# Optimization experiments

Measured on AMD Instinct MI355X. Metric: run time of the kernel, lower is better.

Reference implementation:

```python
import jax, jax.numpy as jnp
import numpy as np

B, H, N, D = 1, 1, 4096, 1024
DFF = 4096
LN_EPS = 1e-5


def _layer_norm(x, g, b):
    m = jnp.mean(x, axis=-1, keepdims=True)
    v = jnp.mean(jnp.square(x - m), axis=-1, keepdims=True)
    return (x - m) * jax.lax.rsqrt(v + LN_EPS) * g + b


def _mha(q, k, v, W, b):
    # NOTE: source has no 1/sqrt(d) scaling -- kept faithful.
    a = jnp.einsum('bhnd,bhmd->bhnm', q, k)
    a = jax.nn.softmax(a, axis=-1)
    o = jnp.einsum('bhnm,bhmd->bhnd', a, v)
    bb, hh, nn, dd = o.shape
    o = o.transpose(0, 2, 1, 3).reshape(bb, nn, hh * dd)  # b n (h d)
    return o @ W.T + b


def setup_inputs() -> dict:
    key = jax.random.key(0)
    ks = jax.random.split(key, 16)
    s = 0.02
    return {
        'x': jax.random.normal(ks[0], (B, H, N, D), jnp.float32),
        'x_encoder': jax.random.normal(ks[1], (B, H, N, D), jnp.float32),
        'pos': jax.random.normal(ks[2], (B, H, N, D), jnp.float32),
        'query_pos': jax.random.normal(ks[3], (B, H, N, D), jnp.float32),
        'Wp_sa': jax.random.normal(ks[4], (D, D), jnp.float32) * s,
        'bp_sa': jnp.zeros((D,), jnp.float32),
        'Wp_ca': jax.random.normal(ks[5], (D, D), jnp.float32) * s,
        'bp_ca': jnp.zeros((D,), jnp.float32),
        'W1': jax.random.normal(ks[6], (DFF, D), jnp.float32) * s,
        'b1': jnp.zeros((DFF,), jnp.float32),
        'W2': jax.random.normal(ks[7], (D, DFF), jnp.float32) * s,
        'b2': jnp.zeros((D,), jnp.float32),
        'g_sa': jnp.ones((D,), jnp.float32),
        'be_sa': jnp.zeros((D,), jnp.float32),
        'g_ca': jnp.ones((D,), jnp.float32),
        'be_ca': jnp.zeros((D,), jnp.float32),
        'g_ff': jnp.ones((D,), jnp.float32),
        'be_ff': jnp.zeros((D,), jnp.float32),
    }


def reference(x, x_encoder, pos, query_pos, Wp_sa, bp_sa, Wp_ca, bp_ca,
              W1, b1, W2, b2, g_sa, be_sa, g_ca, be_ca, g_ff, be_ff):
    # self-attention block
    n1 = _layer_norm(x, g_sa, be_sa)
    qk = n1 + pos
    x = _mha(qk, qk, n1, Wp_sa, bp_sa) + x
    # cross-attention block
    n2 = _layer_norm(x, g_ca, be_ca)
    q = n2 + query_pos
    k = x_encoder + pos
    x = _mha(q, k, x_encoder, Wp_ca, bp_ca) + x
    # feed-forward block (exact GELU, matching torch nn.GELU default)
    n3 = _layer_norm(x, g_ff, be_ff)
    h = jax.nn.gelu(n3 @ W1.T + b1, approximate=False)
    x = (h @ W2.T + b2) + x
    return x
```

## Files before the change

kernel.cpp:

```cpp
#include <hip/hip_runtime.h>
#include <hip/hip_fp16.h>
#include <cstdint>
#include <cstdio>

#define NROW 4096
#define DMODEL 1024
#define DFF_ 4096

typedef _Float16 f16;
typedef _Float16 f16x4 __attribute__((ext_vector_type(4)));
typedef _Float16 f16x8 __attribute__((ext_vector_type(8)));
typedef float f32x4 __attribute__((ext_vector_type(4)));

__device__ __forceinline__ void g2l16(const void* g, void* l) {
  __builtin_amdgcn_global_load_lds((const __attribute__((address_space(1))) void*)g,
                                   (__attribute__((address_space(3))) void*)l,
                                   16, 0, 0);
}

__device__ __forceinline__ int xcd_swz16() {
  const int bid = blockIdx.y * gridDim.x + blockIdx.x;
  const int nwg = gridDim.x * gridDim.y;
  return (bid & 7) * (nwg >> 3) + (bid >> 3);
}

__global__ __launch_bounds__(256) void cvt_f32_f16(const float* __restrict__ in,
                                                   f16* __restrict__ out, long n4) {
  for (long i = (long)blockIdx.x * blockDim.x + threadIdx.x; i < n4;
       i += (long)gridDim.x * blockDim.x) {
    float4 a = ((const float4*)in)[i];
    f16x4 h = {(f16)a.x, (f16)a.y, (f16)a.z, (f16)a.w};
    ((f16x4*)out)[i] = h;
  }
}

__global__ __launch_bounds__(256) void add_cvt(const float* __restrict__ xe,
                                               const float* __restrict__ pos,
                                               f16* __restrict__ k16,
                                               f16* __restrict__ xe16, long n4) {
  for (long i = (long)blockIdx.x * blockDim.x + threadIdx.x; i < n4;
       i += (long)gridDim.x * blockDim.x) {
    float4 a = ((const float4*)xe)[i];
    float4 p = ((const float4*)pos)[i];
    f16x4 k = {(f16)(a.x + p.x), (f16)(a.y + p.y), (f16)(a.z + p.z), (f16)(a.w + p.w)};
    f16x4 v = {(f16)a.x, (f16)a.y, (f16)a.z, (f16)a.w};
    ((f16x4*)k16)[i] = k;
    ((f16x4*)xe16)[i] = v;
  }
}

__global__ __launch_bounds__(256) void ln_row(const float* __restrict__ x,
                                              const float* __restrict__ g,
                                              const float* __restrict__ b,
                                              const float* __restrict__ pos,
                                              f16* __restrict__ nout,
                                              f16* __restrict__ qout) {
  const int row = blockIdx.x, tid = threadIdx.x;
  const float4 xv = ((const float4*)(x + (long)row * DMODEL))[tid];
  float s = xv.x + xv.y + xv.z + xv.w;
  float ss = xv.x * xv.x + xv.y * xv.y + xv.z * xv.z + xv.w * xv.w;
  for (int o = 32; o; o >>= 1) { s += __shfl_xor(s, o); ss += __shfl_xor(ss, o); }
  __shared__ float rs[4], rss[4];
  const int wid = tid >> 6, lane = tid & 63;
  if (!lane) { rs[wid] = s; rss[wid] = ss; }
  __syncthreads();
  s = rs[0] + rs[1] + rs[2] + rs[3];
  ss = rss[0] + rss[1] + rss[2] + rss[3];
  const float mean = s * (1.f / DMODEL);
  const float var = ss * (1.f / DMODEL) - mean * mean;
  const float rstd = rsqrtf(var + 1e-5f);
  const float4 gv = ((const float4*)g)[tid];
  const float4 bv = ((const float4*)b)[tid];
  float4 nv;
  nv.x = (xv.x - mean) * rstd * gv.x + bv.x;
  nv.y = (xv.y - mean) * rstd * gv.y + bv.y;
  nv.z = (xv.z - mean) * rstd * gv.z + bv.z;
  nv.w = (xv.w - mean) * rstd * gv.w + bv.w;
  if (nout) {
    f16x4 h = {(f16)nv.x, (f16)nv.y, (f16)nv.z, (f16)nv.w};
    *(f16x4*)&nout[(long)row * DMODEL + tid * 4] = h;
  }
  float4 pv = {0.f, 0.f, 0.f, 0.f};
  if (pos) pv = ((const float4*)(pos + (long)row * DMODEL))[tid];
  f16x4 q = {(f16)(nv.x + pv.x), (f16)(nv.y + pv.y), (f16)(nv.z + pv.z), (f16)(nv.w + pv.w)};
  *(f16x4*)&qout[(long)row * DMODEL + tid * 4] = q;
}

__global__ __launch_bounds__(256) void softmax_row(const float* __restrict__ S,
                                                   f16* __restrict__ P) {
  const int row = blockIdx.x, tid = threadIdx.x;
  const float4* Sr = (const float4*)(S + (long)row * NROW);
  float4 v[4];
  float m = -1e30f;
#pragma unroll
  for (int i = 0; i < 4; i++) {
    v[i] = Sr[tid + i * 256];
    m = fmaxf(m, fmaxf(fmaxf(v[i].x, v[i].y), fmaxf(v[i].z, v[i].w)));
  }
  for (int o = 32; o; o >>= 1) m = fmaxf(m, __shfl_xor(m, o));
  __shared__ float red[4], red2[4];
  const int wid = tid >> 6, lane = tid & 63;
  if (!lane) red[wid] = m;
  __syncthreads();
  m = fmaxf(fmaxf(red[0], red[1]), fmaxf(red[2], red[3]));
  float sum = 0.f;
#pragma unroll
  for (int i = 0; i < 4; i++) {
    v[i].x = __expf(v[i].x - m); v[i].y = __expf(v[i].y - m);
    v[i].z = __expf(v[i].z - m); v[i].w = __expf(v[i].w - m);
    sum += v[i].x + v[i].y + v[i].z + v[i].w;
  }
  for (int o = 32; o; o >>= 1) sum += __shfl_xor(sum, o);
  if (!lane) red2[wid] = sum;
  __syncthreads();
  sum = red2[0] + red2[1] + red2[2] + red2[3];
  const float r = 1.f / sum;
  f16* Pr = P + (long)row * NROW;
#pragma unroll
  for (int i = 0; i < 4; i++) {
    f16x4 h = {(f16)(v[i].x * r), (f16)(v[i].y * r), (f16)(v[i].z * r), (f16)(v[i].w * r)};
    *(f16x4*)&Pr[(tid + i * 256) * 4] = h;
  }
}

__global__ __launch_bounds__(256) void transpose_h(const f16* __restrict__ in,
                                                   f16* __restrict__ out, int R, int C) {
  __shared__ f16 t[64][72];
  const int tid = threadIdx.x;
  const int r0 = blockIdx.y * 64, c0 = blockIdx.x * 64;
  const int tr = tid >> 4, tc = (tid & 15) * 4;
#pragma unroll
  for (int rr = 0; rr < 4; rr++) {
    int row = rr * 16 + tr;
    f16x4 v = *(const f16x4*)&in[(long)(r0 + row) * C + c0 + tc];
    *(f16x4*)&t[row][tc] = v;
  }
  __syncthreads();
#pragma unroll
  for (int rr = 0; rr < 4; rr++) {
    int row = rr * 16 + tr;
    f16x4 o = {t[tc + 0][row], t[tc + 1][row], t[tc + 2][row], t[tc + 3][row]};
    *(f16x4*)&out[(long)(c0 + row) * R + r0 + tc] = o;
  }
}

enum { EPI_F32 = 0, EPI_F16 = 1, EPI_PROJ = 2, EPI_GELU = 3, EPI_FINAL = 4 };

#define VM4 asm volatile("s_waitcnt vmcnt(4)" ::: "memory")
#define VM0 asm volatile("s_waitcnt vmcnt(0)" ::: "memory")
#define NOP (void)0

#define PH(MQ, NQ, RDA, ASP, RDB, BSP, STG, WAITC)                                 \
  {                                                                                \
    if (RDA) {                                                                     \
      _Pragma("unroll") for (int m = 0; m < 4; ++m) {                              \
        av[m][0] = *(const f16x8*)&(ASP)[arow + m * 1024 + x0];                    \
        av[m][1] = *(const f16x8*)&(ASP)[arow + m * 1024 + x1];                    \
      }                                                                            \
    }                                                                              \
    if (RDB) {                                                                     \
      _Pragma("unroll") for (int n = 0; n < 2; ++n) {                              \
        bv[n][0] = *(const f16x8*)&(BSP)[brow + n * 1024 + x0];                    \
        bv[n][1] = *(const f16x8*)&(BSP)[brow + n * 1024 + x1];                    \
      }                                                                            \
    }                                                                              \
    STG;                                                                           \
    __builtin_amdgcn_sched_barrier(0);                                             \
    WAITC;                                                                         \
    __builtin_amdgcn_s_barrier();                                                  \
    __builtin_amdgcn_s_setprio(1);                                                 \
    _Pragma("unroll") for (int m = 0; m < 4; ++m)                                  \
      _Pragma("unroll") for (int n = 0; n < 2; ++n)                                \
        _Pragma("unroll") for (int kk = 0; kk < 2; ++kk)                           \
          acc[MQ][NQ][m][n] = __builtin_amdgcn_mfma_f32_16x16x32_f16(              \
              av[m][kk], bv[n][kk], acc[MQ][NQ][m][n], 0, 0, 0);                   \
    __builtin_amdgcn_s_setprio(0);                                                 \
    __builtin_amdgcn_sched_barrier(0);                                             \
  }

template <int EPI>
__global__ __launch_bounds__(512) void gemm256(const f16* __restrict__ A,
                                               const f16* __restrict__ B, int K,
                                               void* __restrict__ Cout, int ldc,
                                               const float* __restrict__ bias) {
  __shared__ f16 As[4][128 * 64];
  __shared__ f16 Bs[4][128 * 64];
  const int tid = threadIdx.x;
  const int wid = tid >> 6, lane = tid & 63;
  const int wr = wid >> 2, wc = wid & 3;
  const int lr = lane & 15, lk4 = lane >> 4;
  const int swz = xcd_swz16();
  const long bm = (long)(swz >> 4) * 256, bn = (long)(swz & 15) * 256;
  const f16* Abase = A + bm * K;
  const f16* Bbase = B + bn * K;
  const int nkt = K >> 6;

  const int x0 = (lk4 ^ (lr & 7)) << 3;
  const int x1 = ((4 | lk4) ^ (lr & 7)) << 3;
  const int arow = (wr * 64 + lr) * 64;
  const int brow = (wc * 32 + lr) * 64;

  const int erow0 = tid >> 3;
  const long swo = (long)(((tid & 7) ^ (erow0 & 7)) << 3);
  const f16* sA0 = Abase + (long)erow0 * K + swo;
  const f16* sA1 = sA0 + (long)64 * K;
  const f16* sAh0 = sA0 + (long)128 * K;
  const f16* sAh1 = sA1 + (long)128 * K;
  const f16* sB0 = Bbase + (long)erow0 * K + swo;
  const f16* sB1 = sB0 + (long)64 * K;
  const f16* sBh0 = sB0 + (long)128 * K;
  const f16* sBh1 = sB1 + (long)128 * K;
  const int dlo = tid * 8, dhi = 4096 + tid * 8;

  auto stage2 = [&](const f16* s0, const f16* s1, int k0, f16* dst) {
    g2l16(s0 + k0, dst + dlo);
    g2l16(s1 + k0, dst + dhi);
  };

  f32x4 acc[2][2][4][2];
#pragma unroll
  for (int a = 0; a < 2; ++a)
#pragma unroll
    for (int b = 0; b < 2; ++b)
#pragma unroll
      for (int m = 0; m < 4; ++m)
#pragma unroll
        for (int n = 0; n < 2; ++n) acc[a][b][m][n] = f32x4{0.f, 0.f, 0.f, 0.f};

  f16x8 av[4][2], bv[2][2];

  stage2(sA0, sA1, 0, As[0]);
  stage2(sBh0, sBh1, 0, Bs[1]);
  stage2(sB0, sB1, 0, Bs[0]);
  stage2(sAh0, sAh1, 0, As[1]);
  stage2(sA0, sA1, 64, As[2]);
  stage2(sB0, sB1, 64, Bs[2]);
  __builtin_amdgcn_sched_barrier(0);
  VM4;
  __builtin_amdgcn_s_barrier();
  __builtin_amdgcn_sched_barrier(0);

  int t = 0;
  for (; t <= nkt - 4; t += 2) {
    PH(0, 1, 1, As[0], 1, Bs[1], stage2(sBh0, sBh1, (t + 1) * 64, Bs[3]), NOP)
    PH(0, 0, 0, As[0], 1, Bs[0], stage2(sAh0, sAh1, (t + 1) * 64, As[3]), NOP)
    PH(1, 0, 1, As[1], 0, Bs[0], stage2(sA0, sA1, (t + 2) * 64, As[0]), NOP)
    PH(1, 1, 0, As[1], 1, Bs[1], stage2(sB0, sB1, (t + 2) * 64, Bs[0]), VM4)
    PH(0, 1, 1, As[2], 1, Bs[3], stage2(sBh0, sBh1, (t + 2) * 64, Bs[1]), NOP)
    PH(0, 0, 0, As[2], 1, Bs[2], stage2(sAh0, sAh1, (t + 2) * 64, As[1]), NOP)
    PH(1, 0, 1, As[3], 0, Bs[2], stage2(sA0, sA1, (t + 3) * 64, As[2]), NOP)
    PH(1, 1, 0, As[3], 1, Bs[3], stage2(sB0, sB1, (t + 3) * 64, Bs[2]), VM4)
  }
  PH(0, 1, 1, As[0], 1, Bs[1], stage2(sBh0, sBh1, (nkt - 1) * 64, Bs[3]), NOP)
  PH(0, 0, 0, As[0], 1, Bs[0], stage2(sAh0, sAh1, (nkt - 1) * 64, As[3]), NOP)
  PH(1, 0, 1, As[1], 0, Bs[0], NOP, NOP)
  PH(1, 1, 0, As[1], 1, Bs[1], NOP, VM0)
  PH(0, 1, 1, As[2], 1, Bs[3], NOP, NOP)
  PH(0, 0, 0, As[2], 1, Bs[2], NOP, NOP)
  PH(1, 0, 1, As[3], 0, Bs[2], NOP, NOP)
  PH(1, 1, 0, As[3], 1, Bs[3], NOP, NOP)

  const int l4 = lane >> 4, lf = lane & 15;
#pragma unroll
  for (int mq = 0; mq < 2; ++mq)
#pragma unroll
    for (int nq = 0; nq < 2; ++nq)
#pragma unroll
      for (int m = 0; m < 4; ++m)
#pragma unroll
        for (int n = 0; n < 2; ++n) {
          const long r = bm + mq * 128 + wr * 64 + m * 16 + l4 * 4;
          const long cc = bn + nq * 128 + wc * 32 + n * 16 + lf;
          float bcol = 0.f;
          if (EPI == EPI_GELU) bcol = bias[cc];
#pragma unroll
          for (int q = 0; q < 4; ++q) {
            const long idx = (r + q) * ldc + cc;
            const float v = acc[mq][nq][m][n][q];
            if (EPI == EPI_F32) {
              ((float*)Cout)[idx] = v;
            } else {
              const float h = v + bcol;
              ((f16*)Cout)[idx] = (f16)(0.5f * h * (1.f + erff(h * 0.70710678118654752f)));
            }
          }
        }
}

template <int BN, int BK>
__device__ __forceinline__ void stage_tile(const f16* __restrict__ Arow,
                                           const f16* __restrict__ Brow, int K, int kt,
                                           int tid, f16* Asd, f16* Bsd) {
  constexpr int CH = BK / 8;
  const int k0 = kt * BK;
#pragma unroll
  for (int rr = 0; rr < 128 * CH / 256; ++rr) {
    int e = rr * 256 + tid;
    int row = e / CH, c = e % CH;
    int cs = c ^ (row & (CH - 1));
    g2l16(Arow + (long)row * K + k0 + cs * 8, Asd + e * 8);
  }
#pragma unroll
  for (int rr = 0; rr < BN * CH / 256; ++rr) {
    int e = rr * 256 + tid;
    int row = e / CH, c = e % CH;
    int cs = c ^ (row & (CH - 1));
    g2l16(Brow + (long)row * K + k0 + cs * 8, Bsd + e * 8);
  }
  __builtin_amdgcn_sched_barrier(0);
}

template <int NJ, int BK>
__device__ __forceinline__ void compute_tile(const f16* Asd, const f16* Bsd, int wm,
                                             int wn, int lr, int lk4,
                                             f32x4 (&acc)[4][NJ]) {
  constexpr int CH = BK / 8;
#pragma unroll
  for (int s = 0; s < BK / 32; ++s) {
    const int g = s * 4 + lk4;
    f16x8 av[4], bv[NJ];
#pragma unroll
    for (int i = 0; i < 4; i++) {
      int row = wm + i * 16 + lr;
      int slot = g ^ (row & (CH - 1));
      av[i] = *(const f16x8*)&Asd[row * BK + slot * 8];
    }
#pragma unroll
    for (int j = 0; j < NJ; j++) {
      int row = wn + j * 16 + lr;
      int slot = g ^ (row & (CH - 1));
      bv[j] = *(const f16x8*)&Bsd[row * BK + slot * 8];
    }
#pragma unroll
    for (int i = 0; i < 4; i++)
#pragma unroll
      for (int j = 0; j < NJ; j++)
        acc[i][j] = __builtin_amdgcn_mfma_f32_16x16x32_f16(av[i], bv[j], acc[i][j], 0, 0, 0);
  }
}

template <int EPI, int BN, int BK>
__global__ __launch_bounds__(256) void gemm_nt(const f16* __restrict__ A,
                                               const f16* __restrict__ B, int K,
                                               void* __restrict__ Cout, int ldc,
                                               const float* __restrict__ bias,
                                               const float* __restrict__ res) {
  constexpr int NJ = BN / 32;
  __shared__ f16 As0[128 * BK];
  __shared__ f16 As1[128 * BK];
  __shared__ f16 Bs0[BN * BK];
  __shared__ f16 Bs1[BN * BK];
  const int tid = threadIdx.x;
  const int wid = tid >> 6, lane = tid & 63;
  const int wm = (wid >> 1) * 64, wn = (wid & 1) * (BN / 2);
  const int lr = lane & 15, lk4 = lane >> 4;
  const int swz = xcd_swz16();
  const long bm = (long)(swz >> 4) * 128;
  const long bn = (long)(swz & 15) * BN;

  f32x4 zero = {0.f, 0.f, 0.f, 0.f};
  f32x4 acc[4][NJ];
#pragma unroll
  for (int i = 0; i < 4; i++)
#pragma unroll
    for (int j = 0; j < NJ; j++) acc[i][j] = zero;

  const f16* Arow = A + bm * K;
  const f16* Brow = B + bn * K;
  const int nkt = K / BK;

  stage_tile<BN, BK>(Arow, Brow, K, 0, tid, As0, Bs0);
  __syncthreads();

  int kt = 0;
  for (; kt + 2 < nkt; kt += 2) {
    stage_tile<BN, BK>(Arow, Brow, K, kt + 1, tid, As1, Bs1);
    compute_tile<NJ, BK>(As0, Bs0, wm, wn, lr, lk4, acc);
    __syncthreads();
    stage_tile<BN, BK>(Arow, Brow, K, kt + 2, tid, As0, Bs0);
    compute_tile<NJ, BK>(As1, Bs1, wm, wn, lr, lk4, acc);
    __syncthreads();
  }
  stage_tile<BN, BK>(Arow, Brow, K, nkt - 1, tid, As1, Bs1);
  compute_tile<NJ, BK>(As0, Bs0, wm, wn, lr, lk4, acc);
  __syncthreads();
  compute_tile<NJ, BK>(As1, Bs1, wm, wn, lr, lk4, acc);

  const int r0 = (int)bm + wm + (lane >> 4) * 4;
  const int c0 = (int)bn + wn + (lane & 15);
#pragma unroll
  for (int i = 0; i < 4; i++) {
#pragma unroll
    for (int j = 0; j < NJ; j++) {
      const int c = c0 + j * 16;
      float bcol = 0.f;
      if (EPI == EPI_PROJ || EPI == EPI_GELU || EPI == EPI_FINAL) bcol = bias[c];
#pragma unroll
      for (int q = 0; q < 4; q++) {
        const int r = r0 + i * 16 + q;
        const long idx = (long)r * ldc + c;
        const float v = acc[i][j][q];
        if (EPI == EPI_F32) {
          ((float*)Cout)[idx] = v;
        } else if (EPI == EPI_F16) {
          ((f16*)Cout)[idx] = (f16)v;
        } else if (EPI == EPI_PROJ || EPI == EPI_FINAL) {
          ((float*)Cout)[idx] = v + bcol + res[idx];
        } else {
          const float h = v + bcol;
          const float gg = 0.5f * h * (1.f + erff(h * 0.70710678118654752f));
          ((f16*)Cout)[idx] = (f16)gg;
        }
      }
    }
  }
}

extern "C" void kernel_launch(void* const* d_in, const int* in_sizes, int n_in,
                              void* d_out, int out_size, void* d_ws, size_t ws_size,
                              hipStream_t stream) {
  const float* x = (const float*)d_in[0];
  const float* x_encoder = (const float*)d_in[1];
  const float* pos = (const float*)d_in[2];
  const float* query_pos = (const float*)d_in[3];
  const float* Wp_sa = (const float*)d_in[4];
  const float* bp_sa = (const float*)d_in[5];
  const float* Wp_ca = (const float*)d_in[6];
  const float* bp_ca = (const float*)d_in[7];
  const float* W1 = (const float*)d_in[8];
  const float* b1 = (const float*)d_in[9];
  const float* W2 = (const float*)d_in[10];
  const float* b2 = (const float*)d_in[11];
  const float* g_sa = (const float*)d_in[12];
  const float* be_sa = (const float*)d_in[13];
  const float* g_ca = (const float*)d_in[14];
  const float* be_ca = (const float*)d_in[15];
  const float* g_ff = (const float*)d_in[16];
  const float* be_ff = (const float*)d_in[17];

  const size_t MB = 1024 * 1024;
  char* ws = (char*)d_ws;
  f16* wpsa16 = (f16*)(ws + 0 * MB);
  f16* wpca16 = (f16*)(ws + 2 * MB);
  f16* w116 = (f16*)(ws + 4 * MB);
  f16* w216 = (f16*)(ws + 12 * MB);
  f16* q16 = (f16*)(ws + 20 * MB);
  f16* k16 = (f16*)(ws + 28 * MB);
  f16* n16 = (f16*)(ws + 36 * MB);
  f16* vT = (f16*)(ws + 44 * MB);
  f16* o16 = (f16*)(ws + 52 * MB);
  float* x1 = (float*)(ws + 60 * MB);
  float* x2 = (float*)(ws + 76 * MB);
  float* scores = (float*)(ws + 92 * MB);
  f16* h16 = (f16*)(ws + 92 * MB);
  f16* P16 = (f16*)(ws + 156 * MB);

  if (ws_size < (size_t)188 * MB) {
    fprintf(stderr, "kernel_launch: ws too small (%zu bytes, need %zu)\n", ws_size,
            (size_t)188 * MB);
    return;
  }

  cvt_f32_f16<<<1024, 256, 0, stream>>>(Wp_sa, wpsa16, (long)DMODEL * DMODEL / 4);
  cvt_f32_f16<<<1024, 256, 0, stream>>>(Wp_ca, wpca16, (long)DMODEL * DMODEL / 4);
  cvt_f32_f16<<<2048, 256, 0, stream>>>(W1, w116, (long)DFF_ * DMODEL / 4);
  cvt_f32_f16<<<2048, 256, 0, stream>>>(W2, w216, (long)DMODEL * DFF_ / 4);

  ln_row<<<NROW, 256, 0, stream>>>(x, g_sa, be_sa, pos, n16, q16);
  transpose_h<<<dim3(DMODEL / 64, NROW / 64), 256, 0, stream>>>(n16, vT, NROW, DMODEL);
  gemm256<EPI_F32><<<dim3(16, 16), 512, 0, stream>>>(q16, q16, DMODEL, scores, NROW,
                                                     nullptr);
  softmax_row<<<NROW, 256, 0, stream>>>(scores, P16);
  gemm_nt<EPI_F16, 64, 64><<<dim3(16, 32), 256, 0, stream>>>(P16, vT, NROW, o16, DMODEL,
                                                             nullptr, nullptr);
  gemm_nt<EPI_PROJ, 64, 64><<<dim3(16, 32), 256, 0, stream>>>(o16, wpsa16, DMODEL, x1,
                                                              DMODEL, bp_sa, x);

  ln_row<<<NROW, 256, 0, stream>>>(x1, g_ca, be_ca, query_pos, nullptr, q16);
  add_cvt<<<2048, 256, 0, stream>>>(x_encoder, pos, k16, n16, (long)NROW * DMODEL / 4);
  transpose_h<<<dim3(DMODEL / 64, NROW / 64), 256, 0, stream>>>(n16, vT, NROW, DMODEL);
  gemm256<EPI_F32><<<dim3(16, 16), 512, 0, stream>>>(q16, k16, DMODEL, scores, NROW,
                                                     nullptr);
  softmax_row<<<NROW, 256, 0, stream>>>(scores, P16);
  gemm_nt<EPI_F16, 64, 64><<<dim3(16, 32), 256, 0, stream>>>(P16, vT, NROW, o16, DMODEL,
                                                             nullptr, nullptr);
  gemm_nt<EPI_PROJ, 64, 64><<<dim3(16, 32), 256, 0, stream>>>(o16, wpca16, DMODEL, x2,
                                                              DMODEL, bp_ca, x1);

  ln_row<<<NROW, 256, 0, stream>>>(x2, g_ff, be_ff, nullptr, nullptr, q16);
  gemm256<EPI_GELU><<<dim3(16, 16), 512, 0, stream>>>(q16, w116, DMODEL, h16, DFF_, b1);
  gemm_nt<EPI_FINAL, 64, 64><<<dim3(16, 32), 256, 0, stream>>>(h16, w216, DFF_,
                                                               (float*)d_out, DMODEL, b2,
                                                               x2);
}
```

Measured before the change: 387.4 us.

## Software-pipeline LDS fragment reads one phase ahead in 256x256 GEMM

Restructures the 8-phase GEMM main loop so LDS reads of A/B fragments for the next phase are issued before the current phase's MFMAs, using double-buffered register fragments (avA0/avA1, bvB0, bv1a/bv1b). The barrier moves to the start of each phase, and the vmcnt waits become vmcnt(2) at different points. The aim is to hide LDS read latency behind MFMA work. The cost is extra VGPR pressure and a more fragile synchronisation schedule that could hurt occupancy or correctness.

Measured after the change: 458.1 us. 18.3% more time.

```diff
diff --git a/kernel.cpp b/kernel.cpp
--- a/kernel.cpp
+++ b/kernel.cpp
@@ -147,35 +147,45 @@
 enum { EPI_F32 = 0, EPI_F16 = 1, EPI_PROJ = 2, EPI_GELU = 3, EPI_FINAL = 4 };
 
 #define VM4 asm volatile("s_waitcnt vmcnt(4)" ::: "memory")
+#define VM2 asm volatile("s_waitcnt vmcnt(2)" ::: "memory")
 #define VM0 asm volatile("s_waitcnt vmcnt(0)" ::: "memory")
 #define NOP (void)0
 
-#define PH(MQ, NQ, RDA, ASP, RDB, BSP, STG, WAITC)                                 \
+#define RA(dst, ASP)                                             \
+  {                                                              \
+    _Pragma("unroll") for (int m = 0; m < 4; ++m) {              \
+      dst[m][0] = *(const f16x8*)&(ASP)[arow + m * 1024 + x0];   \
+      dst[m][1] = *(const f16x8*)&(ASP)[arow + m * 1024 + x1];   \
+    }                                                            \
+  }
+#define RB(dst, BSP)                                             \
+  {                                                              \
+    _Pragma("unroll") for (int n = 0; n < 2; ++n) {              \
+      dst[n][0] = *(const f16x8*)&(BSP)[brow + n * 1024 + x0];   \
+      dst[n][1] = *(const f16x8*)&(BSP)[brow + n * 1024 + x1];   \
+    }                                                            \
+  }
+#define RAB(adst, ASP, bdst, BSP)                                \
+  {                                                              \
+    RA(adst, ASP);                                               \
+    RB(bdst, BSP);                                               \
+  }
+
+#define PH3(MQ, NQ, AV, BV, RDS, STG, ENDW)                                        \
   {                                                                                \
-    if (RDA) {                                                                     \
-      _Pragma("unroll") for (int m = 0; m < 4; ++m) {                              \
-        av[m][0] = *(const f16x8*)&(ASP)[arow + m * 1024 + x0];                    \
-        av[m][1] = *(const f16x8*)&(ASP)[arow + m * 1024 + x1];                    \
-      }                                                                            \
-    }                                                                              \
-    if (RDB) {                                                                     \
-      _Pragma("unroll") for (int n = 0; n < 2; ++n) {                              \
-        bv[n][0] = *(const f16x8*)&(BSP)[brow + n * 1024 + x0];                    \
-        bv[n][1] = *(const f16x8*)&(BSP)[brow + n * 1024 + x1];                    \
-      }                                                                            \
-    }                                                                              \
+    __builtin_amdgcn_s_barrier();                                                  \
+    __builtin_amdgcn_sched_barrier(0);                                             \
+    RDS;                                                                           \
     STG;                                                                           \
-    __builtin_amdgcn_sched_barrier(0);                                             \
-    WAITC;                                                                         \
-    __builtin_amdgcn_s_barrier();                                                  \
     __builtin_amdgcn_s_setprio(1);                                                 \
     _Pragma("unroll") for (int m = 0; m < 4; ++m)                                  \
       _Pragma("unroll") for (int n = 0; n < 2; ++n)                                \
         _Pragma("unroll") for (int kk = 0; kk < 2; ++kk)                           \
           acc[MQ][NQ][m][n] = __builtin_amdgcn_mfma_f32_16x16x32_f16(              \
-              av[m][kk], bv[n][kk], acc[MQ][NQ][m][n], 0, 0, 0);                   \
+              AV[m][kk], BV[n][kk], acc[MQ][NQ][m][n], 0, 0, 0);                   \
     __builtin_amdgcn_s_setprio(0);                                                 \
     __builtin_amdgcn_sched_barrier(0);                                             \
+    ENDW;                                                                          \
   }
 
 template <int EPI>
@@ -227,7 +237,7 @@
 #pragma unroll
         for (int n = 0; n < 2; ++n) acc[a][b][m][n] = f32x4{0.f, 0.f, 0.f, 0.f};
 
-  f16x8 av[4][2], bv[2][2];
+  f16x8 avA0[4][2], avA1[4][2], bvB0[2][2], bv1a[2][2], bv1b[2][2];
 
   stage2(sA0, sA1, 0, As[0]);
   stage2(sBh0, sBh1, 0, Bs[1]);
@@ -239,26 +249,30 @@
   VM4;
   __builtin_amdgcn_s_barrier();
   __builtin_amdgcn_sched_barrier(0);
+  RA(avA0, As[0]);
+  RB(bv1a, Bs[1]);
 
   int t = 0;
-  for (; t <= nkt - 4; t += 2) {
-    PH(0, 1, 1, As[0], 1, Bs[1], stage2(sBh0, sBh1, (t + 1) * 64, Bs[3]), NOP)
-    PH(0, 0, 0, As[0], 1, Bs[0], stage2(sAh0, sAh1, (t + 1) * 64, As[3]), NOP)
-    PH(1, 0, 1, As[1], 0, Bs[0], stage2(sA0, sA1, (t + 2) * 64, As[0]), NOP)
-    PH(1, 1, 0, As[1], 1, Bs[1], stage2(sB0, sB1, (t + 2) * 64, Bs[0]), VM4)
-    PH(0, 1, 1, As[2], 1, Bs[3], stage2(sBh0, sBh1, (t + 2) * 64, Bs[1]), NOP)
-    PH(0, 0, 0, As[2], 1, Bs[2], stage2(sAh0, sAh1, (t + 2) * 64, As[1]), NOP)
-    PH(1, 0, 1, As[3], 0, Bs[2], stage2(sA0, sA1, (t + 3) * 64, As[2]), NOP)
-    PH(1, 1, 0, As[3], 1, Bs[3], stage2(sB0, sB1, (t + 3) * 64, Bs[2]), VM4)
-  }
-  PH(0, 1, 1, As[0], 1, Bs[1], stage2(sBh0, sBh1, (nkt - 1) * 64, Bs[3]), NOP)
-  PH(0, 0, 0, As[0], 1, Bs[0], stage2(sAh0, sAh1, (nkt - 1) * 64, As[3]), NOP)
-  PH(1, 0, 1, As[1], 0, Bs[0], NOP, NOP)
-  PH(1, 1, 0, As[1], 1, Bs[1], NOP, VM0)
-  PH(0, 1, 1, As[2], 1, Bs[3], NOP, NOP)
-  PH(0, 0, 0, As[2], 1, Bs[2], NOP, NOP)
-  PH(1, 0, 1, As[3], 0, Bs[2], NOP, NOP)
-  PH(1, 1, 0, As[3], 1, Bs[3], NOP, NOP)
+  for (; t + 2 < nkt; t += 2) {
+    PH3(0, 1, avA0, bv1a, RB(bvB0, Bs[0]), stage2(sBh0, sBh1, (t + 1) * 64, Bs[3]), NOP)
+    PH3(0, 0, avA0, bvB0, RA(avA1, As[1]), stage2(sAh0, sAh1, (t + 1) * 64, As[3]), NOP)
+    PH3(1, 0, avA1, bvB0, NOP, stage2(sA0, sA1, (t + 2) * 64, As[0]), VM2)
+    PH3(1, 1, avA1, bv1a, RAB(avA0, As[2], bv1b, Bs[3]),
+        stage2(sB0, sB1, (t + 2) * 64, Bs[0]), NOP)
+    PH3(0, 1, avA0, bv1b, RB(bvB0, Bs[2]), stage2(sBh0, sBh1, (t + 2) * 64, Bs[1]), NOP)
+    PH3(0, 0, avA0, bvB0, RA(avA1, As[3]), stage2(sAh0, sAh1, (t + 2) * 64, As[1]), NOP)
+    PH3(1, 0, avA1, bvB0, NOP, stage2(sA0, sA1, (t + 3) * 64, As[2]), VM2)
+    PH3(1, 1, avA1, bv1b, RAB(avA0, As[0], bv1a, Bs[1]),
+        stage2(sB0, sB1, (t + 3) * 64, Bs[2]), NOP)
+  }
+  PH3(0, 1, avA0, bv1a, RB(bvB0, Bs[0]), stage2(sBh0, sBh1, (nkt - 1) * 64, Bs[3]), NOP)
+  PH3(0, 0, avA0, bvB0, RA(avA1, As[1]), stage2(sAh0, sAh1, (nkt - 1) * 64, As[3]), NOP)
+  PH3(1, 0, avA1, bvB0, NOP, NOP, VM0)
+  PH3(1, 1, avA1, bv1a, RAB(avA0, As[2], bv1b, Bs[3]), NOP, NOP)
+  PH3(0, 1, avA0, bv1b, RB(bvB0, Bs[2]), NOP, NOP)
+  PH3(0, 0, avA0, bvB0, RA(avA1, As[3]), NOP, NOP)
+  PH3(1, 0, avA1, bvB0, NOP, NOP, NOP)
+  PH3(1, 1, avA1, bv1b, NOP, NOP, NOP)
 
   const int l4 = lane >> 4, lf = lane & 15;
 #pragma unroll
```

## Fuse softmax into score GEMM epilogue stats and PV GEMM prologue

Applied to the files above, without the earlier changes.

The standalone softmax pass is removed. The QK^T GEMM epilogue now also emits partial row max and exp-sum for each 64-column slice. A tiny kernel reduces these into per-row max and reciprocal sum. A new PV GEMM reads the fp32 scores directly, applies exp and normalisation while staging A into LDS, and multiplies by V^T. This drops one full read and write of the 4096x4096 score matrix and the fp16 P buffer, at the cost of recomputing exp inside the GEMM and loading fp32 A through registers rather than async LDS loads.

Result: slower. 473.0 us (+22.1%).

```diff
diff --git a/kernel.cpp b/kernel.cpp
--- a/kernel.cpp
+++ b/kernel.cpp
@@ -86,43 +86,6 @@
   *(f16x4*)&qout[(long)row * DMODEL + tid * 4] = q;
 }
 
-__global__ __launch_bounds__(256) void softmax_row(const float* __restrict__ S,
-                                                   f16* __restrict__ P) {
-  const int row = blockIdx.x, tid = threadIdx.x;
-  const float4* Sr = (const float4*)(S + (long)row * NROW);
-  float4 v[4];
-  float m = -1e30f;
-#pragma unroll
-  for (int i = 0; i < 4; i++) {
-    v[i] = Sr[tid + i * 256];
-    m = fmaxf(m, fmaxf(fmaxf(v[i].x, v[i].y), fmaxf(v[i].z, v[i].w)));
-  }
-  for (int o = 32; o; o >>= 1) m = fmaxf(m, __shfl_xor(m, o));
-  __shared__ float red[4], red2[4];
-  const int wid = tid >> 6, lane = tid & 63;
-  if (!lane) red[wid] = m;
-  __syncthreads();
-  m = fmaxf(fmaxf(red[0], red[1]), fmaxf(red[2], red[3]));
-  float sum = 0.f;
-#pragma unroll
-  for (int i = 0; i < 4; i++) {
-    v[i].x = __expf(v[i].x - m); v[i].y = __expf(v[i].y - m);
-    v[i].z = __expf(v[i].z - m); v[i].w = __expf(v[i].w - m);
-    sum += v[i].x + v[i].y + v[i].z + v[i].w;
-  }
-  for (int o = 32; o; o >>= 1) sum += __shfl_xor(sum, o);
-  if (!lane) red2[wid] = sum;
-  __syncthreads();
-  sum = red2[0] + red2[1] + red2[2] + red2[3];
-  const float r = 1.f / sum;
-  f16* Pr = P + (long)row * NROW;
-#pragma unroll
-  for (int i = 0; i < 4; i++) {
-    f16x4 h = {(f16)(v[i].x * r), (f16)(v[i].y * r), (f16)(v[i].z * r), (f16)(v[i].w * r)};
-    *(f16x4*)&Pr[(tid + i * 256) * 4] = h;
-  }
-}
-
 __global__ __launch_bounds__(256) void transpose_h(const f16* __restrict__ in,
                                                    f16* __restrict__ out, int R, int C) {
   __shared__ f16 t[64][72];
@@ -142,6 +105,18 @@
     f16x4 o = {t[tc + 0][row], t[tc + 1][row], t[tc + 2][row], t[tc + 3][row]};
     *(f16x4*)&out[(long)(c0 + row) * R + r0 + tc] = o;
   }
+}
+
+__global__ __launch_bounds__(256) void reduce_stats(const float2* __restrict__ pb,
+                                                    float2* __restrict__ st) {
+  const int row = blockIdx.x * 4 + (threadIdx.x >> 6);
+  const int lane = threadIdx.x & 63;
+  float2 p = pb[(long)row * 64 + lane];
+  float mx = p.x;
+  for (int off = 1; off < 64; off <<= 1) mx = fmaxf(mx, __shfl_xor(mx, off));
+  float s = p.y * __expf(p.x - mx);
+  for (int off = 1; off < 64; off <<= 1) s += __shfl_xor(s, off);
+  if (!lane) st[row] = make_float2(mx, 1.f / s);
 }
 
 enum { EPI_F32 = 0, EPI_F16 = 1, EPI_PROJ = 2, EPI_GELU = 3, EPI_FINAL = 4 };
@@ -182,7 +157,8 @@
 __global__ __launch_bounds__(512) void gemm256(const f16* __restrict__ A,
                                                const f16* __restrict__ B, int K,
                                                void* __restrict__ Cout, int ldc,
-                                               const float* __restrict__ bias) {
+                                               const float* __restrict__ bias,
+                                               float2* __restrict__ pb) {
   __shared__ f16 As[4][128 * 64];
   __shared__ f16 Bs[4][128 * 64];
   const int tid = threadIdx.x;
@@ -285,6 +261,26 @@
             }
           }
         }
+
+  if (EPI == EPI_F32) {
+#pragma unroll
+    for (int mq = 0; mq < 2; ++mq)
+#pragma unroll
+      for (int m = 0; m < 4; ++m)
+#pragma unroll
+        for (int q = 0; q < 4; ++q) {
+          const float v0 = acc[mq][0][m][0][q], v1 = acc[mq][0][m][1][q];
+          const float v2 = acc[mq][1][m][0][q], v3 = acc[mq][1][m][1][q];
+          float mx = fmaxf(fmaxf(v0, v1), fmaxf(v2, v3));
+          for (int off = 1; off < 16; off <<= 1) mx = fmaxf(mx, __shfl_xor(mx, off, 16));
+          float sm = __expf(v0 - mx) + __expf(v1 - mx) + __expf(v2 - mx) + __expf(v3 - mx);
+          for (int off = 1; off < 16; off <<= 1) sm += __shfl_xor(sm, off, 16);
+          if (lf == 0) {
+            const long r = bm + mq * 128 + wr * 64 + m * 16 + l4 * 4 + q;
+            pb[r * 64 + (swz & 15) * 4 + wc] = make_float2(mx, sm);
+          }
+        }
+  }
 }
 
 template <int BN, int BK>
@@ -414,6 +410,121 @@
       }
     }
   }
+}
+
+__global__ __launch_bounds__(256) void gemm_pv(const float* __restrict__ S,
+                                               const float2* __restrict__ st,
+                                               const f16* __restrict__ B,
+                                               f16* __restrict__ Cout) {
+  constexpr int BK = 64, BN = 64, NJ = 2;
+  __shared__ f16 As0[128 * 64];
+  __shared__ f16 As1[128 * 64];
+  __shared__ f16 Bs0[64 * 64];
+  __shared__ f16 Bs1[64 * 64];
+  const int tid = threadIdx.x;
+  const int wid = tid >> 6, lane = tid & 63;
+  const int wm = (wid >> 1) * 64, wn = (wid & 1) * 32;
+  const int lr = lane & 15, lk4 = lane >> 4;
+  const int swz = xcd_swz16();
+  const long bm = (long)(swz >> 4) * 128;
+  const long bn = (long)(swz & 15) * BN;
+
+  const int arow_ = tid >> 3, ac = tid & 7;
+  const int cs = ac ^ (arow_ & 7);
+  const float* srcA[4];
+  float2 strow[4];
+#pragma unroll
+  for (int rr = 0; rr < 4; ++rr) {
+    const int row = rr * 32 + arow_;
+    srcA[rr] = S + (long)(bm + row) * NROW + cs * 8;
+    strow[rr] = st[bm + row];
+  }
+  const f16* srcB0 = B + (long)(bn + arow_) * NROW + cs * 8;
+  const f16* srcB1 = srcB0 + (long)32 * NROW;
+  const int dB0 = tid * 8, dB1 = 2048 + tid * 8;
+
+  auto stageB = [&](int k0, f16* Bsd) {
+    g2l16(srcB0 + k0, Bsd + dB0);
+    g2l16(srcB1 + k0, Bsd + dB1);
+  };
+
+  float4 ra[4][2];
+  auto loadA = [&](int k0) {
+#pragma unroll
+    for (int rr = 0; rr < 4; ++rr) {
+      ra[rr][0] = *(const float4*)(srcA[rr] + k0);
+      ra[rr][1] = *(const float4*)(srcA[rr] + k0 + 4);
+    }
+  };
+  auto writeA = [&](f16* Asd) {
+#pragma unroll
+    for (int rr = 0; rr < 4; ++rr) {
+      const float m = strow[rr].x, ri = strow[rr].y;
+      f16x8 h;
+      h[0] = (f16)(__expf(ra[rr][0].x - m) * ri);
+      h[1] = (f16)(__expf(ra[rr][0].y - m) * ri);
+      h[2] = (f16)(__expf(ra[rr][0].z - m) * ri);
+      h[3] = (f16)(__expf(ra[rr][0].w - m) * ri);
+      h[4] = (f16)(__expf(ra[rr][1].x - m) * ri);
+      h[5] = (f16)(__expf(ra[rr][1].y - m) * ri);
+      h[6] = (f16)(__expf(ra[rr][1].z - m) * ri);
+      h[7] = (f16)(__expf(ra[rr][1].w - m) * ri);
+      *(f16x8*)&Asd[(rr * 256 + tid) * 8] = h;
+    }
+  };
+
+  f32x4 acc[4][NJ];
+#pragma unroll
+  for (int i = 0; i < 4; i++)
+#pragma unroll
+    for (int j = 0; j < NJ; j++) acc[i][j] = f32x4{0.f, 0.f, 0.f, 0.f};
+
+  const int nkt = NROW / BK;
+
+  loadA(0);
+  stageB(0, Bs0);
+  __builtin_amdgcn_sched_barrier(0);
+  asm volatile("s_waitcnt vmcnt(2)" ::: "memory");
+  writeA(As0);
+  __syncthreads();
+
+  int kt = 0;
+  for (; kt + 2 < nkt; kt += 2) {
+    loadA((kt + 1) * BK);
+    stageB((kt + 1) * BK, Bs1);
+    __builtin_amdgcn_sched_barrier(0);
+    compute_tile<NJ, BK>(As0, Bs0, wm, wn, lr, lk4, acc);
+    asm volatile("s_waitcnt vmcnt(2)" ::: "memory");
+    writeA(As1);
+    __syncthreads();
+    loadA((kt + 2) * BK);
+    stageB((kt + 2) * BK, Bs0);
+    __builtin_amdgcn_sched_barrier(0);
+    compute_tile<NJ, BK>(As1, Bs1, wm, wn, lr, lk4, acc);
+    asm volatile("s_waitcnt vmcnt(2)" ::: "memory");
+    writeA(As0);
+    __syncthreads();
+  }
+  loadA((nkt - 1) * BK);
+  stageB((nkt - 1) * BK, Bs1);
+  __builtin_amdgcn_sched_barrier(0);
+  compute_tile<NJ, BK>(As0, Bs0, wm, wn, lr, lk4, acc);
+  asm volatile("s_waitcnt vmcnt(2)" ::: "memory");
+  writeA(As1);
+  __syncthreads();
+  compute_tile<NJ, BK>(As1, Bs1, wm, wn, lr, lk4, acc);
+
+  const int r0 = (int)bm + wm + (lane >> 4) * 4;
+  const int c0 = (int)bn + wn + (lane & 15);
+#pragma unroll
+  for (int i = 0; i < 4; i++)
+#pragma unroll
+    for (int j = 0; j < NJ; j++)
+#pragma unroll
+      for (int q = 0; q < 4; q++) {
+        const int r = r0 + i * 16 + q;
+        Cout[(long)r * DMODEL + c0 + j * 16] = (f16)acc[i][j][q];
+      }
 }
 
 extern "C" void kernel_launch(void* const* d_in, const int* in_sizes, int n_in,
@@ -453,11 +564,12 @@
   float* x2 = (float*)(ws + 76 * MB);
   float* scores = (float*)(ws + 92 * MB);
   f16* h16 = (f16*)(ws + 92 * MB);
-  f16* P16 = (f16*)(ws + 156 * MB);
-
-  if (ws_size < (size_t)188 * MB) {
+  float2* pb = (float2*)(ws + 156 * MB);
+  float2* st = (float2*)(ws + 158 * MB);
+
+  if (ws_size < (size_t)160 * MB) {
     fprintf(stderr, "kernel_launch: ws too small (%zu bytes, need %zu)\n", ws_size,
-            (size_t)188 * MB);
+            (size_t)160 * MB);
     return;
   }
 
@@ -469,10 +581,9 @@
   ln_row<<<NROW, 256, 0, stream>>>(x, g_sa, be_sa, pos, n16, q16);
   transpose_h<<<dim3(DMODEL / 64, NROW / 64), 256, 0, stream>>>(n16, vT, NROW, DMODEL);
   gemm256<EPI_F32><<<dim3(16, 16), 512, 0, stream>>>(q16, q16, DMODEL, scores, NROW,
-                                                     nullptr);
-  softmax_row<<<NROW, 256, 0, stream>>>(scores, P16);
-  gemm_nt<EPI_F16, 64, 64><<<dim3(16, 32), 256, 0, stream>>>(P16, vT, NROW, o16, DMODEL,
-                                                             nullptr, nullptr);
+                                                     nullptr, pb);
+  reduce_stats<<<1024, 256, 0, stream>>>(pb, st);
+  gemm_pv<<<dim3(16, 32), 256, 0, stream>>>(scores, st, vT, o16);
   gemm_nt<EPI_PROJ, 64, 64><<<dim3(16, 32), 256, 0, stream>>>(o16, wpsa16, DMODEL, x1,
                                                               DMODEL, bp_sa, x);
 
@@ -480,15 +591,15 @@
   add_cvt<<<2048, 256, 0, stream>>>(x_encoder, pos, k16, n16, (long)NROW * DMODEL / 4);
   transpose_h<<<dim3(DMODEL / 64, NROW / 64), 256, 0, stream>>>(n16, vT, NROW, DMODEL);
   gemm256<EPI_F32><<<dim3(16, 16), 512, 0, stream>>>(q16, k16, DMODEL, scores, NROW,
-                                                     nullptr);
-  softmax_row<<<NROW, 256, 0, stream>>>(scores, P16);
-  gemm_nt<EPI_F16, 64, 64><<<dim3(16, 32), 256, 0, stream>>>(P16, vT, NROW, o16, DMODEL,
-                                                             nullptr, nullptr);
+                                                     nullptr, pb);
+  reduce_stats<<<1024, 256, 0, stream>>>(pb, st);
+  gemm_pv<<<dim3(16, 32), 256, 0, stream>>>(scores, st, vT, o16);
   gemm_nt<EPI_PROJ, 64, 64><<<dim3(16, 32), 256, 0, stream>>>(o16, wpca16, DMODEL, x2,
                                                               DMODEL, bp_ca, x1);
 
   ln_row<<<NROW, 256, 0, stream>>>(x2, g_ff, be_ff, nullptr, nullptr, q16);
-  gemm256<EPI_GELU><<<dim3(16, 16), 512, 0, stream>>>(q16, w116, DMODEL, h16, DFF_, b1);
+  gemm256<EPI_GELU><<<dim3(16, 16), 512, 0, stream>>>(q16, w116, DMODEL, h16, DFF_, b1,
+                                                      nullptr);
   gemm_nt<EPI_FINAL, 64, 64><<<dim3(16, 32), 256, 0, stream>>>(h16, w216, DFF_,
                                                                (float*)d_out, DMODEL, b2,
                                                                x2);
```
